# Performance work log

Measured on AMD Instinct MI355X. Metric: run time of the kernel, lower is better.

## Reference

```python
import jax, jax.numpy as jnp
import numpy as np

D_MODEL = 1024
N_HEADS = 16
D_FF = 4096
D_K = D_MODEL // N_HEADS


def _ln(x, g, b, eps=1e-5):
    mu = jnp.mean(x, axis=-1, keepdims=True)
    var = jnp.mean(jnp.square(x - mu), axis=-1, keepdims=True)
    return (x - mu) * jax.lax.rsqrt(var + eps) * g + b


def setup_inputs() -> dict:
    key = jax.random.key(0)
    ks = jax.random.split(key, 16)
    s = 0.02
    inp = {
        "x": jax.random.normal(ks[0], (2, 2048, D_MODEL), dtype=jnp.float32),
        "Wq": jax.random.normal(ks[1], (D_MODEL, D_MODEL), dtype=jnp.float32) * s,
        "bq": jnp.zeros((D_MODEL,), jnp.float32),
        "Wk": jax.random.normal(ks[2], (D_MODEL, D_MODEL), dtype=jnp.float32) * s,
        "bk": jnp.zeros((D_MODEL,), jnp.float32),
        "Wv": jax.random.normal(ks[3], (D_MODEL, D_MODEL), dtype=jnp.float32) * s,
        "bv": jnp.zeros((D_MODEL,), jnp.float32),
        "Wo": jax.random.normal(ks[4], (D_MODEL, D_MODEL), dtype=jnp.float32) * s,
        "bo": jnp.zeros((D_MODEL,), jnp.float32),
        "W1": jax.random.normal(ks[5], (D_MODEL, D_FF), dtype=jnp.float32) * s,
        "b1": jnp.zeros((D_FF,), jnp.float32),
        "W2": jax.random.normal(ks[6], (D_FF, D_MODEL), dtype=jnp.float32) * s,
        "b2": jnp.zeros((D_MODEL,), jnp.float32),
        "g1": jnp.ones((D_MODEL,), jnp.float32),
        "be1": jnp.zeros((D_MODEL,), jnp.float32),
        "g2": jnp.ones((D_MODEL,), jnp.float32),
        "be2": jnp.zeros((D_MODEL,), jnp.float32),
    }
    return inp


def reference(x, Wq, bq, Wk, bk, Wv, bv, Wo, bo, W1, b1, W2, b2, g1, be1, g2, be2):
    B, L, D = x.shape
    # QKV projections -> [B, H, L, d_k]
    q = (x @ Wq + bq).reshape(B, L, N_HEADS, D_K).transpose(0, 2, 1, 3)
    k = (x @ Wk + bk).reshape(B, L, N_HEADS, D_K).transpose(0, 2, 1, 3)
    v = (x @ Wv + bv).reshape(B, L, N_HEADS, D_K).transpose(0, 2, 1, 3)
    scores = jnp.einsum("bhqd,bhkd->bhqk", q, k) / jnp.sqrt(jnp.float32(D_K))
    attn = jax.nn.softmax(scores, axis=-1)
    ctx = jnp.einsum("bhqk,bhkd->bhqd", attn, v)
    ctx = ctx.transpose(0, 2, 1, 3).reshape(B, L, D)
    attn_out = ctx @ Wo + bo
    # residual + LN1
    h = _ln(x + attn_out, g1, be1)
    # FFN (exact GELU, matching torch F.gelu default)
    ff = jax.nn.gelu(h @ W1 + b1, approximate=False) @ W2 + b2
    return _ln(h + ff, g2, be2)
```

## Files before the change

kernel.cpp:

```cpp
#include <hip/hip_runtime.h>
#include <cmath>


typedef unsigned short u16;
typedef unsigned int u32;
typedef __attribute__((ext_vector_type(8))) __bf16 bf16x8;
typedef __attribute__((ext_vector_type(4))) float f32x4;

#define MFMA16(a, b, c) __builtin_amdgcn_mfma_f32_16x16x32_bf16(a, b, c, 0, 0, 0)

__device__ __forceinline__ u16 f2bf(float f) {
  u32 u = __builtin_bit_cast(u32, f);
  u += 0x7fffu + ((u >> 16) & 1u);
  return (u16)(u >> 16);
}

__device__ __forceinline__ u32 packtrunc(float lo, float hi) {
#if __has_builtin(__builtin_amdgcn_perm)
  return __builtin_amdgcn_perm(__builtin_bit_cast(u32, hi),
                               __builtin_bit_cast(u32, lo), 0x07060302u);
#else
  return (__builtin_bit_cast(u32, lo) >> 16) |
         (__builtin_bit_cast(u32, hi) & 0xFFFF0000u);
#endif
}

__device__ __forceinline__ bf16x8 ld_frag(const u16* p) {
  return __builtin_bit_cast(bf16x8, *(const uint4*)p);
}

__device__ __forceinline__ float fexp2(float x) {
#if __has_builtin(__builtin_amdgcn_exp2f)
  return __builtin_amdgcn_exp2f(x);
#else
  return exp2f(x);
#endif
}

__device__ __forceinline__ void gload16(const u16* g, u16* l) {
  __builtin_amdgcn_global_load_lds(
      (const __attribute__((address_space(1))) void*)g,
      (__attribute__((address_space(3))) void*)l, 16, 0, 0);
}

__global__ __launch_bounds__(256) void cvt_bf16_k(const float* __restrict__ src,
                                                  u16* __restrict__ dst) {
  int i = (blockIdx.x * 256 + threadIdx.x) * 4;
  float4 v = *(const float4*)(src + i);
  ushort4 o;
  o.x = f2bf(v.x); o.y = f2bf(v.y); o.z = f2bf(v.z); o.w = f2bf(v.w);
  *(ushort4*)(dst + i) = o;
}

__global__ __launch_bounds__(256) void transpose_bf16_k(const float* __restrict__ src,
                                                        u16* __restrict__ dst,
                                                        int R, int C) {
  __shared__ float tile[32][33];
  int tx = threadIdx.x & 31, ty = threadIdx.x >> 5;
  int c0 = blockIdx.x * 32, r0 = blockIdx.y * 32;
#pragma unroll
  for (int i = 0; i < 4; i++)
    tile[ty + 8 * i][tx] = src[(long)(r0 + ty + 8 * i) * C + c0 + tx];
  __syncthreads();
#pragma unroll
  for (int i = 0; i < 4; i++)
    dst[(long)(c0 + ty + 8 * i) * R + r0 + tx] = f2bf(tile[tx][ty + 8 * i]);
}

__global__ __launch_bounds__(256) void transpose4_bf16_k(
    const float* __restrict__ Wq, const float* __restrict__ Wk,
    const float* __restrict__ Wv, const float* __restrict__ Wo,
    u16* __restrict__ wqkvT, u16* __restrict__ woT) {
  const int z = blockIdx.z;
  const float* src = (z == 0) ? Wq : (z == 1) ? Wk : (z == 2) ? Wv : Wo;
  u16* dst = (z < 3) ? (wqkvT + (size_t)z * 1024 * 1024) : woT;
  __shared__ float tile[32][33];
  int tx = threadIdx.x & 31, ty = threadIdx.x >> 5;
  int c0 = blockIdx.x * 32, r0 = blockIdx.y * 32;
#pragma unroll
  for (int i = 0; i < 4; i++)
    tile[ty + 8 * i][tx] = src[(long)(r0 + ty + 8 * i) * 1024 + c0 + tx];
  __syncthreads();
#pragma unroll
  for (int i = 0; i < 4; i++)
    dst[(long)(c0 + ty + 8 * i) * 1024 + r0 + tx] = f2bf(tile[tx][ty + 8 * i]);
}

template <int MODE, int TN>
__global__ __launch_bounds__(256) void gemm_k(
    const u16* __restrict__ A, const u16* __restrict__ BT, int M, int N, int K,
    const float* __restrict__ bias, float* __restrict__ outF, u16* __restrict__ outB,
    u16* __restrict__ qd, u16* __restrict__ kd, u16* __restrict__ vTd,
    const float* __restrict__ bq, const float* __restrict__ bk, const float* __restrict__ bv) {
  constexpr int NT = TN / 32;
  __shared__ u16 As[2][128 * 32];
  __shared__ u16 Bs[2][TN * 32];
  const int tid = threadIdx.x;
  const int wave = tid >> 6, lane = tid & 63, quad = lane >> 4, l16 = lane & 15;
  const int wm = wave >> 1, wn = wave & 1;
  const int m0 = blockIdx.y * 128, n0 = blockIdx.x * TN;

  const int srow = lane >> 2;
  const int sxor = (lane & 3) ^ (srow & 3);
  const u16* aS0 = A + (long)(m0 + wave * 32 + srow) * K + sxor * 8;
  const u16* aS1 = aS0 + 16 * K;
  const u16* bS0 = BT + (long)(n0 + (TN == 128 ? wave * 32 : wave * 16) + srow) * K + sxor * 8;
  const u16* bS1 = bS0 + 16 * K;

  int aoff[4], boff[NT];
#pragma unroll
  for (int t = 0; t < 4; t++) {
    int ra = wm * 64 + t * 16 + l16;
    aoff[t] = ra * 32 + ((quad ^ (l16 & 3)) * 8);
  }
#pragma unroll
  for (int t = 0; t < NT; t++) {
    int rb = wn * (TN / 2) + t * 16 + l16;
    boff[t] = rb * 32 + ((quad ^ (l16 & 3)) * 8);
  }

  auto stage = [&](int buf, int k0) {
    gload16(aS0 + k0, &As[buf][(wave * 2 + 0) * 512]);
    gload16(aS1 + k0, &As[buf][(wave * 2 + 1) * 512]);
    if (TN == 128) {
      gload16(bS0 + k0, &Bs[buf][(wave * 2 + 0) * 512]);
      gload16(bS1 + k0, &Bs[buf][(wave * 2 + 1) * 512]);
    } else {
      gload16(bS0 + k0, &Bs[buf][wave * 512]);
    }
  };

  f32x4 acc[4][NT] = {};

  stage(0, 0);
#pragma unroll 1
  for (int k0 = 0; k0 < K; k0 += 32) {
    const int buf = (k0 >> 5) & 1;
    __syncthreads();
    if (k0 + 32 < K) stage(buf ^ 1, k0 + 32);
    bf16x8 af[4], bfr[NT];
#pragma unroll
    for (int t = 0; t < 4; t++) af[t] = ld_frag(&As[buf][aoff[t]]);
#pragma unroll
    for (int t = 0; t < NT; t++) bfr[t] = ld_frag(&Bs[buf][boff[t]]);
#pragma unroll
    for (int mt = 0; mt < 4; mt++)
#pragma unroll
      for (int nt = 0; nt < NT; nt++)
        acc[mt][nt] = MFMA16(af[mt], bfr[nt], acc[mt][nt]);
  }

  if (MODE == 0) {
    const int nbase = n0 + wn * (TN / 2);
    const int mat = nbase >> 10;
    const float* bp = (mat == 0) ? bq : ((mat == 1) ? bk : bv);
    float bb[NT];
    int hh0[NT], dd0[NT];
#pragma unroll
    for (int nt = 0; nt < NT; nt++) {
      int nn = (nbase + nt * 16 + l16) & 1023;
      bb[nt] = bp[nn];
      hh0[nt] = nn >> 6;
      dd0[nt] = nn & 63;
    }
    if (mat < 2) {
#pragma unroll
      for (int mt = 0; mt < 4; mt++) {
#pragma unroll
        for (int r = 0; r < 4; r++) {
          int mr = m0 + wm * 64 + mt * 16 + quad * 4 + r;
          int bI = mr >> 11, ll = mr & 2047;
#pragma unroll
          for (int nt = 0; nt < NT; nt++) {
            float v = acc[mt][nt][r] + bb[nt];
            long idx = ((long)((bI * 16 + hh0[nt]) * 2048 + ll)) * 64 + dd0[nt];
            if (mat == 0) {
              qd[idx] = f2bf(v * 0.18033688011112043f);
            } else {
              kd[idx] = f2bf(v);
            }
          }
        }
      }
    } else {
#pragma unroll
      for (int nt = 0; nt < NT; nt++) {
#pragma unroll
        for (int mt = 0; mt < 4; mt++) {
#pragma unroll
          for (int r = 0; r < 4; r++) {
            int mr = m0 + wm * 64 + mt * 16 + quad * 4 + r;
            int bI = mr >> 11, ll = mr & 2047;
            float v = acc[mt][nt][r] + bb[nt];
            vTd[((long)((bI * 16 + hh0[nt]) * 64 + dd0[nt])) * 2048 + ll] = f2bf(v);
          }
        }
      }
    }
  } else if (MODE == 1) {
    float bb[NT];
#pragma unroll
    for (int nt = 0; nt < NT; nt++) bb[nt] = bias[n0 + wn * (TN / 2) + nt * 16 + l16];
#pragma unroll
    for (int mt = 0; mt < 4; mt++) {
#pragma unroll
      for (int r = 0; r < 4; r++) {
        int mr = m0 + wm * 64 + mt * 16 + quad * 4 + r;
        float* orow = outF + (long)mr * N + n0 + wn * (TN / 2) + l16;
#pragma unroll
        for (int nt = 0; nt < NT; nt++)
          orow[nt * 16] = acc[mt][nt][r] + bb[nt];
      }
    }
  } else {
    float bb[NT];
#pragma unroll
    for (int nt = 0; nt < NT; nt++) bb[nt] = bias[n0 + wn * (TN / 2) + nt * 16 + l16];
#pragma unroll
    for (int mt = 0; mt < 4; mt++) {
#pragma unroll
      for (int r = 0; r < 4; r++) {
        int mr = m0 + wm * 64 + mt * 16 + quad * 4 + r;
        u16* orow = outB + (long)mr * N + n0 + wn * (TN / 2) + l16;
#pragma unroll
        for (int nt = 0; nt < NT; nt++) {
          float v = acc[mt][nt][r] + bb[nt];
          v = 0.5f * v * (1.0f + erff(v * 0.70710678118654752f));
          orow[nt * 16] = f2bf(v);
        }
      }
    }
  }
}

__global__ __launch_bounds__(256) void attn_k(const u16* __restrict__ qd,
                                              const u16* __restrict__ kd,
                                              const u16* __restrict__ vTd,
                                              u16* __restrict__ ctx) {
  __shared__ u16 Ks[2][64 * 64];
  __shared__ u16 Vs[2][64 * 64];
  __shared__ __align__(16) u16 P[4][32][72];
  const int tid = threadIdx.x;
  const int wave = tid >> 6, lane = tid & 63, quad = lane >> 4, l16 = lane & 15;
  const int bh = blockIdx.y;
  const u16* Q = qd + (long)bh * 2048 * 64;
  const u16* Kp = kd + (long)bh * 2048 * 64;
  const u16* Vt = vTd + (long)bh * 64 * 2048;
  const int qbase = blockIdx.x * 128 + wave * 32;

  bf16x8 qf[2][2];
#pragma unroll
  for (int qs = 0; qs < 2; qs++) {
    qf[qs][0] = ld_frag(Q + (qbase + qs * 16 + l16) * 64 + quad * 8);
    qf[qs][1] = ld_frag(Q + (qbase + qs * 16 + l16) * 64 + 32 + quad * 8);
  }

  f32x4 o[2][4] = {};
  float m[2] = {-1e30f, -1e30f}, l[2] = {0.f, 0.f};

  const int srow = lane >> 3;
  const int sx = (lane & 7) ^ srow;
  const int kr0 = wave * 16 + srow;
  const int kr1 = wave * 16 + 8 + srow;

  const int fs0 = ((0 * 4 + quad) ^ (l16 & 7)) * 8;
  const int fs1 = ((1 * 4 + quad) ^ (l16 & 7)) * 8;

  auto stage = [&](int buf, int j0) {
    gload16(Kp + (long)(j0 + kr0) * 64 + sx * 8, &Ks[buf][(wave * 2 + 0) * 512]);
    gload16(Kp + (long)(j0 + kr1) * 64 + sx * 8, &Ks[buf][(wave * 2 + 1) * 512]);
    gload16(Vt + (long)kr0 * 2048 + j0 + sx * 8, &Vs[buf][(wave * 2 + 0) * 512]);
    gload16(Vt + (long)kr1 * 2048 + j0 + sx * 8, &Vs[buf][(wave * 2 + 1) * 512]);
  };

  stage(0, 0);

#pragma unroll 1
  for (int j0 = 0; j0 < 2048; j0 += 64) {
    const int buf = (j0 >> 6) & 1;
    __syncthreads();
    if (j0 + 64 < 2048) stage(buf ^ 1, j0 + 64);

    const u16* kb = &Ks[buf][0];
    f32x4 st[2][4];
#pragma unroll
    for (int f = 0; f < 4; f++) {
      bf16x8 k0 = ld_frag(kb + (f * 16 + l16) * 64 + fs0);
      bf16x8 k1 = ld_frag(kb + (f * 16 + l16) * 64 + fs1);
      f32x4 s0 = {}, s1 = {};
      s0 = MFMA16(k0, qf[0][0], s0); s0 = MFMA16(k1, qf[0][1], s0);
      s1 = MFMA16(k0, qf[1][0], s1); s1 = MFMA16(k1, qf[1][1], s1);
      st[0][f] = s0; st[1][f] = s1;
    }

#pragma unroll
    for (int qs = 0; qs < 2; qs++) {
      float mx = -1e30f;
#pragma unroll
      for (int f = 0; f < 4; f++)
        mx = fmaxf(mx, fmaxf(fmaxf(st[qs][f][0], st[qs][f][1]),
                             fmaxf(st[qs][f][2], st[qs][f][3])));
      mx = fmaxf(mx, __shfl_xor(mx, 16));
      mx = fmaxf(mx, __shfl_xor(mx, 32));
      if (__ballot(mx > m[qs])) {
        float mn = fmaxf(m[qs], mx);
        float al = fexp2(m[qs] - mn);
        m[qs] = mn;
        l[qs] *= al;
#pragma unroll
        for (int nt = 0; nt < 4; nt++) {
          o[qs][nt][0] *= al; o[qs][nt][1] *= al;
          o[qs][nt][2] *= al; o[qs][nt][3] *= al;
        }
      }
      float sm = 0.f;
      u16* prow = &P[wave][qs * 16 + l16][0];
#pragma unroll
      for (int f = 0; f < 4; f++) {
        float p0 = fexp2(st[qs][f][0] - m[qs]);
        float p1 = fexp2(st[qs][f][1] - m[qs]);
        float p2 = fexp2(st[qs][f][2] - m[qs]);
        float p3 = fexp2(st[qs][f][3] - m[qs]);
        sm += (p0 + p1) + (p2 + p3);
        uint2 u;
        u.x = packtrunc(p0, p1);
        u.y = packtrunc(p2, p3);
        *(uint2*)(prow + f * 16 + quad * 4) = u;
      }
      sm += __shfl_xor(sm, 16);
      sm += __shfl_xor(sm, 32);
      l[qs] += sm;
    }
    __asm__ volatile("s_waitcnt lgkmcnt(0)" ::: "memory");

    const u16* vb = &Vs[buf][0];
    bf16x8 vf[4][2];
#pragma unroll
    for (int nt = 0; nt < 4; nt++) {
      vf[nt][0] = ld_frag(vb + (nt * 16 + l16) * 64 + fs0);
      vf[nt][1] = ld_frag(vb + (nt * 16 + l16) * 64 + fs1);
    }
#pragma unroll
    for (int qs = 0; qs < 2; qs++) {
      const u16* prow = &P[wave][qs * 16 + l16][0];
#pragma unroll
      for (int kh = 0; kh < 2; kh++) {
        bf16x8 pf = ld_frag(prow + kh * 32 + quad * 8);
#pragma unroll
        for (int nt = 0; nt < 4; nt++)
          o[qs][nt] = MFMA16(vf[nt][kh], pf, o[qs][nt]);
      }
    }
  }

  const int bI = bh >> 4, hh = bh & 15;
#pragma unroll
  for (int qs = 0; qs < 2; qs++) {
    const float rl = 1.0f / l[qs];
    const long row = (long)(bI * 2048 + qbase + qs * 16 + l16);
#pragma unroll
    for (int nt = 0; nt < 4; nt++) {
      ushort4 w;
      w.x = f2bf(o[qs][nt][0] * rl);
      w.y = f2bf(o[qs][nt][1] * rl);
      w.z = f2bf(o[qs][nt][2] * rl);
      w.w = f2bf(o[qs][nt][3] * rl);
      *(ushort4*)(ctx + row * 1024 + hh * 64 + nt * 16 + quad * 4) = w;
    }
  }
}

__global__ __launch_bounds__(256) void ln_k(const float* __restrict__ a,
                                            const float* __restrict__ b,
                                            const float* __restrict__ g,
                                            const float* __restrict__ be,
                                            float* __restrict__ outF,
                                            u16* __restrict__ outB) {
  const int row = blockIdx.x, tid = threadIdx.x;
  const float* pa = a + (long)row * 1024;
  const float* pb = b + (long)row * 1024;
  float v[4], s = 0.f, sq = 0.f;
#pragma unroll
  for (int i = 0; i < 4; i++) {
    int c = i * 256 + tid;
    v[i] = pa[c] + pb[c];
    s += v[i];
    sq += v[i] * v[i];
  }
#pragma unroll
  for (int off = 1; off < 64; off <<= 1) {
    s += __shfl_xor(s, off);
    sq += __shfl_xor(sq, off);
  }
  __shared__ float red[10];
  int wave = tid >> 6, lane = tid & 63;
  if (lane == 0) { red[wave * 2] = s; red[wave * 2 + 1] = sq; }
  __syncthreads();
  if (tid == 0) {
    float S = red[0] + red[2] + red[4] + red[6];
    float Q = red[1] + red[3] + red[5] + red[7];
    float mu = S * (1.0f / 1024.0f);
    float var = Q * (1.0f / 1024.0f) - mu * mu;
    red[8] = mu;
    red[9] = rsqrtf(var + 1e-5f);
  }
  __syncthreads();
  float mu = red[8], rstd = red[9];
#pragma unroll
  for (int i = 0; i < 4; i++) {
    int c = i * 256 + tid;
    float o = (v[i] - mu) * rstd * g[c] + be[c];
    outF[(long)row * 1024 + c] = o;
    if (outB) outB[(long)row * 1024 + c] = f2bf(o);
  }
}

extern "C" void kernel_launch(void* const* d_in, const int* in_sizes, int n_in,
                              void* d_out, int out_size, void* d_ws, size_t ws_size,
                              hipStream_t stream) {
  const float* x  = (const float*)d_in[0];
  const float* Wq = (const float*)d_in[1];  const float* bq = (const float*)d_in[2];
  const float* Wk = (const float*)d_in[3];  const float* bk = (const float*)d_in[4];
  const float* Wv = (const float*)d_in[5];  const float* bv = (const float*)d_in[6];
  const float* Wo = (const float*)d_in[7];  const float* bo = (const float*)d_in[8];
  const float* W1 = (const float*)d_in[9];  const float* b1 = (const float*)d_in[10];
  const float* W2 = (const float*)d_in[11]; const float* b2 = (const float*)d_in[12];
  const float* g1 = (const float*)d_in[13]; const float* be1 = (const float*)d_in[14];
  const float* g2 = (const float*)d_in[15]; const float* be2 = (const float*)d_in[16];

  char* ws = (char*)d_ws;
  size_t off = 0;
  auto alloc = [&](size_t bytes) {
    size_t o = off;
    off += (bytes + 255) & ~(size_t)255;
    return o;
  };
  u16*   xb     = (u16*)(ws + alloc(4096UL * 1024 * 2));
  u16*   wqkvT  = (u16*)(ws + alloc(3072UL * 1024 * 2));
  u16*   woT    = (u16*)(ws + alloc(1024UL * 1024 * 2));
  u16*   w1T    = (u16*)(ws + alloc(4096UL * 1024 * 2));
  u16*   w2T    = (u16*)(ws + alloc(1024UL * 4096 * 2));
  u16*   qb     = (u16*)(ws + alloc(32UL * 2048 * 64 * 2));
  u16*   kb     = (u16*)(ws + alloc(32UL * 2048 * 64 * 2));
  u16*   vTb    = (u16*)(ws + alloc(32UL * 64 * 2048 * 2));
  u16*   ctx    = (u16*)(ws + alloc(4096UL * 1024 * 2));
  float* attnO  = (float*)(ws + alloc(4096UL * 1024 * 4));
  float* h      = (float*)(ws + alloc(4096UL * 1024 * 4));
  u16*   hb     = (u16*)(ws + alloc(4096UL * 1024 * 2));
  u16*   ff1    = (u16*)(ws + alloc(4096UL * 4096 * 2));
  float* ff2    = (float*)(ws + alloc(4096UL * 1024 * 4));
  if (off > ws_size) return;

  cvt_bf16_k<<<4096, 256, 0, stream>>>(x, xb);
  transpose4_bf16_k<<<dim3(32, 32, 4), 256, 0, stream>>>(Wq, Wk, Wv, Wo, wqkvT, woT);
  transpose_bf16_k<<<dim3(128, 32), 256, 0, stream>>>(W1, w1T, 1024, 4096);
  transpose_bf16_k<<<dim3(32, 128), 256, 0, stream>>>(W2, w2T, 4096, 1024);

  gemm_k<0, 128><<<dim3(24, 32), 256, 0, stream>>>(xb, wqkvT, 4096, 3072, 1024,
                                                   nullptr, nullptr, nullptr,
                                                   qb, kb, vTb, bq, bk, bv);
  attn_k<<<dim3(16, 32), 256, 0, stream>>>(qb, kb, vTb, ctx);
  gemm_k<1, 64><<<dim3(16, 32), 256, 0, stream>>>(ctx, woT, 4096, 1024, 1024,
                                                  bo, attnO, nullptr,
                                                  nullptr, nullptr, nullptr, nullptr, nullptr, nullptr);
  ln_k<<<4096, 256, 0, stream>>>(x, attnO, g1, be1, h, hb);
  gemm_k<2, 128><<<dim3(32, 32), 256, 0, stream>>>(hb, w1T, 4096, 4096, 1024,
                                                   b1, nullptr, ff1,
                                                   nullptr, nullptr, nullptr, nullptr, nullptr, nullptr);
  gemm_k<1, 64><<<dim3(16, 32), 256, 0, stream>>>(ff1, w2T, 4096, 1024, 4096,
                                                  b2, ff2, nullptr,
                                                  nullptr, nullptr, nullptr, nullptr, nullptr, nullptr);
  ln_k<<<4096, 256, 0, stream>>>(h, ff2, g2, be2, (float*)d_out, nullptr);
}
```

Before: 418.9 us.

## Add 256x256 four-stage pipelined GEMM with split-K FFN2 and fused reduction LayerNorm

Adds a 512-thread GEMM kernel with 256x256 output tiles, a 4-deep LDS ring filled by direct global-to-LDS loads with explicit vmcnt waits, and interleaved stage/MFMA with priority bumps. It is used for the QKV projection and FFN1 to raise arithmetic intensity per tile. The FFN2 GEMM becomes split-K over 4 slices, writing partials into reused workspace buffers (ff2, attnO, qb, vTb). A new LayerNorm kernel sums the partials and the bias before normalising. This fixes the occupancy problem that a 4096x1024 output with large tiles would cause, at the cost of extra partial-sum memory traffic. Reusing qb and vTb as scratch relies on their sizes being sufficient.

```diff
diff --git a/kernel.cpp b/kernel.cpp
--- a/kernel.cpp
+++ b/kernel.cpp
@@ -42,6 +42,9 @@
       (const __attribute__((address_space(1))) void*)g,
       (__attribute__((address_space(3))) void*)l, 16, 0, 0);
 }
+
+#define WAITVL(N) asm volatile("s_waitcnt vmcnt(" #N ") lgkmcnt(0)" ::: "memory")
+#define BAR() do { __builtin_amdgcn_s_barrier(); asm volatile("" ::: "memory"); } while (0)
 
 __global__ __launch_bounds__(256) void cvt_bf16_k(const float* __restrict__ src,
                                                   u16* __restrict__ dst) {
@@ -84,6 +87,172 @@
 #pragma unroll
   for (int i = 0; i < 4; i++)
     dst[(long)(c0 + ty + 8 * i) * 1024 + r0 + tx] = f2bf(tile[tx][ty + 8 * i]);
+}
+
+template <int MODE>
+__global__ __launch_bounds__(512, 2) void gemm256_k(
+    const u16* __restrict__ A, const u16* __restrict__ BT,
+    int N, int lda, int ldb, int Kc,
+    const float* __restrict__ bias, float* __restrict__ outF, u16* __restrict__ outB,
+    float* __restrict__ p1, float* __restrict__ p2, float* __restrict__ p3,
+    u16* __restrict__ qd, u16* __restrict__ kd, u16* __restrict__ vTd,
+    const float* __restrict__ bq, const float* __restrict__ bk, const float* __restrict__ bv) {
+  __shared__ u16 As[4][256 * 32];
+  __shared__ u16 Bs[4][256 * 32];
+  const int tid = threadIdx.x;
+  const int wave = tid >> 6, lane = tid & 63, quad = lane >> 4, l16 = lane & 15;
+  const int wm = wave >> 2, wn = wave & 3;
+  const int m0 = blockIdx.y * 256, n0 = blockIdx.x * 256;
+  const int kz = blockIdx.z;
+  const long kofs = (long)kz * Kc;
+  const int KT = Kc >> 5;
+
+  const int srow = lane >> 2;
+  const int sseg = (lane & 3) ^ (srow & 3);
+  const u16* aS = A + (long)(m0 + wave * 32 + srow) * lda + kofs + sseg * 8;
+  const u16* bS = BT + (long)(n0 + wave * 32 + srow) * ldb + kofs + sseg * 8;
+
+  auto stageA = [&](int sb, int s) {
+    const u16* p = aS + (long)s * 32;
+    gload16(p, &As[sb][wave * 1024]);
+    gload16(p + 16 * (long)lda, &As[sb][wave * 1024 + 512]);
+  };
+  auto stageB = [&](int sb, int s) {
+    const u16* p = bS + (long)s * 32;
+    gload16(p, &Bs[sb][wave * 1024]);
+    gload16(p + 16 * (long)ldb, &Bs[sb][wave * 1024 + 512]);
+  };
+
+  int aro[8], bro[4];
+#pragma unroll
+  for (int mf = 0; mf < 8; mf++) {
+    int r = wm * 128 + mf * 16 + l16;
+    aro[mf] = r * 32 + ((quad ^ (r & 3)) * 8);
+  }
+#pragma unroll
+  for (int nf = 0; nf < 4; nf++) {
+    int r = wn * 64 + nf * 16 + l16;
+    bro[nf] = r * 32 + ((quad ^ (r & 3)) * 8);
+  }
+
+  f32x4 acc[8][4] = {};
+
+  stageA(0, 0); stageB(0, 0);
+  stageA(1, 1); stageB(1, 1);
+  stageA(2, 2); stageB(2, 2);
+
+#pragma unroll 1
+  for (int t = 0; t < KT; ++t) {
+    const int buf = t & 3;
+    if (t < KT - 2)      { WAITVL(8); }
+    else if (t == KT - 2){ WAITVL(4); }
+    else                 { WAITVL(0); }
+    BAR();
+
+    if (t + 3 < KT) stageA((t + 3) & 3, t + 3);
+    bf16x8 af[4], bf4[4];
+#pragma unroll
+    for (int i = 0; i < 4; i++) af[i] = ld_frag(&As[buf][aro[i]]);
+#pragma unroll
+    for (int i = 0; i < 4; i++) bf4[i] = ld_frag(&Bs[buf][bro[i]]);
+    __builtin_amdgcn_s_setprio(1);
+#pragma unroll
+    for (int mf = 0; mf < 4; mf++)
+#pragma unroll
+      for (int nf = 0; nf < 4; nf++)
+        acc[mf][nf] = MFMA16(af[mf], bf4[nf], acc[mf][nf]);
+    __builtin_amdgcn_s_setprio(0);
+
+    if (t + 3 < KT) stageB((t + 3) & 3, t + 3);
+#pragma unroll
+    for (int i = 0; i < 4; i++) af[i] = ld_frag(&As[buf][aro[4 + i]]);
+    __builtin_amdgcn_s_setprio(1);
+#pragma unroll
+    for (int mf = 0; mf < 4; mf++)
+#pragma unroll
+      for (int nf = 0; nf < 4; nf++)
+        acc[4 + mf][nf] = MFMA16(af[mf], bf4[nf], acc[4 + mf][nf]);
+    __builtin_amdgcn_s_setprio(0);
+  }
+
+  if (MODE == 0) {
+    const int nbase = n0 + wn * 64;
+    const int mat = nbase >> 10;
+    const float* bp = (mat == 0) ? bq : ((mat == 1) ? bk : bv);
+    float bb[4];
+    int hh0[4], dd0[4];
+#pragma unroll
+    for (int nf = 0; nf < 4; nf++) {
+      int nn = (nbase + nf * 16 + l16) & 1023;
+      bb[nf] = bp[nn];
+      hh0[nf] = nn >> 6;
+      dd0[nf] = nn & 63;
+    }
+    if (mat < 2) {
+#pragma unroll
+      for (int mf = 0; mf < 8; mf++) {
+#pragma unroll
+        for (int r = 0; r < 4; r++) {
+          int mr = m0 + wm * 128 + mf * 16 + quad * 4 + r;
+          int bI = mr >> 11, ll = mr & 2047;
+#pragma unroll
+          for (int nf = 0; nf < 4; nf++) {
+            float v = acc[mf][nf][r] + bb[nf];
+            long idx = ((long)((bI * 16 + hh0[nf]) * 2048 + ll)) * 64 + dd0[nf];
+            if (mat == 0) {
+              qd[idx] = f2bf(v * 0.18033688011112043f);
+            } else {
+              kd[idx] = f2bf(v);
+            }
+          }
+        }
+      }
+    } else {
+#pragma unroll
+      for (int nf = 0; nf < 4; nf++) {
+#pragma unroll
+        for (int mf = 0; mf < 8; mf++) {
+#pragma unroll
+          for (int r = 0; r < 4; r++) {
+            int mr = m0 + wm * 128 + mf * 16 + quad * 4 + r;
+            int bI = mr >> 11, ll = mr & 2047;
+            float v = acc[mf][nf][r] + bb[nf];
+            vTd[((long)((bI * 16 + hh0[nf]) * 64 + dd0[nf])) * 2048 + ll] = f2bf(v);
+          }
+        }
+      }
+    }
+  } else if (MODE == 2) {
+    float bb[4];
+#pragma unroll
+    for (int nf = 0; nf < 4; nf++) bb[nf] = bias[n0 + wn * 64 + nf * 16 + l16];
+#pragma unroll
+    for (int mf = 0; mf < 8; mf++) {
+#pragma unroll
+      for (int r = 0; r < 4; r++) {
+        int mr = m0 + wm * 128 + mf * 16 + quad * 4 + r;
+        u16* orow = outB + (long)mr * N + n0 + wn * 64 + l16;
+#pragma unroll
+        for (int nf = 0; nf < 4; nf++) {
+          float v = acc[mf][nf][r] + bb[nf];
+          v = 0.5f * v * (1.0f + erff(v * 0.70710678118654752f));
+          orow[nf * 16] = f2bf(v);
+        }
+      }
+    }
+  } else {
+    float* sl = (kz == 0) ? outF : (kz == 1) ? p1 : (kz == 2) ? p2 : p3;
+#pragma unroll
+    for (int mf = 0; mf < 8; mf++) {
+#pragma unroll
+      for (int r = 0; r < 4; r++) {
+        int mr = m0 + wm * 128 + mf * 16 + quad * 4 + r;
+        float* orow = sl + (long)mr * N + n0 + wn * 64 + l16;
+#pragma unroll
+        for (int nf = 0; nf < 4; nf++) orow[nf * 16] = acc[mf][nf][r];
+      }
+    }
+  }
 }
 
 template <int MODE, int TN>
@@ -150,54 +319,7 @@
         acc[mt][nt] = MFMA16(af[mt], bfr[nt], acc[mt][nt]);
   }
 
-  if (MODE == 0) {
-    const int nbase = n0 + wn * (TN / 2);
-    const int mat = nbase >> 10;
-    const float* bp = (mat == 0) ? bq : ((mat == 1) ? bk : bv);
-    float bb[NT];
-    int hh0[NT], dd0[NT];
-#pragma unroll
-    for (int nt = 0; nt < NT; nt++) {
-      int nn = (nbase + nt * 16 + l16) & 1023;
-      bb[nt] = bp[nn];
-      hh0[nt] = nn >> 6;
-      dd0[nt] = nn & 63;
-    }
-    if (mat < 2) {
-#pragma unroll
-      for (int mt = 0; mt < 4; mt++) {
-#pragma unroll
-        for (int r = 0; r < 4; r++) {
-          int mr = m0 + wm * 64 + mt * 16 + quad * 4 + r;
-          int bI = mr >> 11, ll = mr & 2047;
-#pragma unroll
-          for (int nt = 0; nt < NT; nt++) {
-            float v = acc[mt][nt][r] + bb[nt];
-            long idx = ((long)((bI * 16 + hh0[nt]) * 2048 + ll)) * 64 + dd0[nt];
-            if (mat == 0) {
-              qd[idx] = f2bf(v * 0.18033688011112043f);
-            } else {
-              kd[idx] = f2bf(v);
-            }
-          }
-        }
-      }
-    } else {
-#pragma unroll
-      for (int nt = 0; nt < NT; nt++) {
-#pragma unroll
-        for (int mt = 0; mt < 4; mt++) {
-#pragma unroll
-          for (int r = 0; r < 4; r++) {
-            int mr = m0 + wm * 64 + mt * 16 + quad * 4 + r;
-            int bI = mr >> 11, ll = mr & 2047;
-            float v = acc[mt][nt][r] + bb[nt];
-            vTd[((long)((bI * 16 + hh0[nt]) * 64 + dd0[nt])) * 2048 + ll] = f2bf(v);
-          }
-        }
-      }
-    }
-  } else if (MODE == 1) {
+  if (MODE == 1) {
     float bb[NT];
 #pragma unroll
     for (int nt = 0; nt < NT; nt++) bb[nt] = bias[n0 + wn * (TN / 2) + nt * 16 + l16];
@@ -210,24 +332,6 @@
 #pragma unroll
         for (int nt = 0; nt < NT; nt++)
           orow[nt * 16] = acc[mt][nt][r] + bb[nt];
-      }
-    }
-  } else {
-    float bb[NT];
-#pragma unroll
-    for (int nt = 0; nt < NT; nt++) bb[nt] = bias[n0 + wn * (TN / 2) + nt * 16 + l16];
-#pragma unroll
-    for (int mt = 0; mt < 4; mt++) {
-#pragma unroll
-      for (int r = 0; r < 4; r++) {
-        int mr = m0 + wm * 64 + mt * 16 + quad * 4 + r;
-        u16* orow = outB + (long)mr * N + n0 + wn * (TN / 2) + l16;
-#pragma unroll
-        for (int nt = 0; nt < NT; nt++) {
-          float v = acc[mt][nt][r] + bb[nt];
-          v = 0.5f * v * (1.0f + erff(v * 0.70710678118654752f));
-          orow[nt * 16] = f2bf(v);
-        }
       }
     }
   }
@@ -412,6 +516,52 @@
     float o = (v[i] - mu) * rstd * g[c] + be[c];
     outF[(long)row * 1024 + c] = o;
     if (outB) outB[(long)row * 1024 + c] = f2bf(o);
+  }
+}
+
+__global__ __launch_bounds__(256) void ln4_k(const float* __restrict__ a,
+                                             const float* __restrict__ q0,
+                                             const float* __restrict__ q1,
+                                             const float* __restrict__ q2,
+                                             const float* __restrict__ q3,
+                                             const float* __restrict__ bias,
+                                             const float* __restrict__ g,
+                                             const float* __restrict__ be,
+                                             float* __restrict__ outF) {
+  const int row = blockIdx.x, tid = threadIdx.x;
+  const long base = (long)row * 1024;
+  float v[4], s = 0.f, sq = 0.f;
+#pragma unroll
+  for (int i = 0; i < 4; i++) {
+    int c = i * 256 + tid;
+    float ff = (q0[base + c] + q1[base + c]) + (q2[base + c] + q3[base + c]) + bias[c];
+    v[i] = a[base + c] + ff;
+    s += v[i];
+    sq += v[i] * v[i];
+  }
+#pragma unroll
+  for (int off = 1; off < 64; off <<= 1) {
+    s += __shfl_xor(s, off);
+    sq += __shfl_xor(sq, off);
+  }
+  __shared__ float red[10];
+  int wave = tid >> 6, lane = tid & 63;
+  if (lane == 0) { red[wave * 2] = s; red[wave * 2 + 1] = sq; }
+  __syncthreads();
+  if (tid == 0) {
+    float S = red[0] + red[2] + red[4] + red[6];
+    float Q = red[1] + red[3] + red[5] + red[7];
+    float mu = S * (1.0f / 1024.0f);
+    float var = Q * (1.0f / 1024.0f) - mu * mu;
+    red[8] = mu;
+    red[9] = rsqrtf(var + 1e-5f);
+  }
+  __syncthreads();
+  float mu = red[8], rstd = red[9];
+#pragma unroll
+  for (int i = 0; i < 4; i++) {
+    int c = i * 256 + tid;
+    outF[base + c] = (v[i] - mu) * rstd * g[c] + be[c];
   }
 }
 
@@ -451,24 +601,32 @@
   float* ff2    = (float*)(ws + alloc(4096UL * 1024 * 4));
   if (off > ws_size) return;
 
+  float* sl0 = ff2;
+  float* sl1 = attnO;
+  float* sl2 = (float*)qb;
+  float* sl3 = (float*)vTb;
+
   cvt_bf16_k<<<4096, 256, 0, stream>>>(x, xb);
   transpose4_bf16_k<<<dim3(32, 32, 4), 256, 0, stream>>>(Wq, Wk, Wv, Wo, wqkvT, woT);
   transpose_bf16_k<<<dim3(128, 32), 256, 0, stream>>>(W1, w1T, 1024, 4096);
   transpose_bf16_k<<<dim3(32, 128), 256, 0, stream>>>(W2, w2T, 4096, 1024);
 
-  gemm_k<0, 128><<<dim3(24, 32), 256, 0, stream>>>(xb, wqkvT, 4096, 3072, 1024,
-                                                   nullptr, nullptr, nullptr,
-                                                   qb, kb, vTb, bq, bk, bv);
+  gemm256_k<0><<<dim3(12, 16), 512, 0, stream>>>(
+      xb, wqkvT, 3072, 1024, 1024, 1024,
+      nullptr, nullptr, nullptr, nullptr, nullptr, nullptr,
+      qb, kb, vTb, bq, bk, bv);
   attn_k<<<dim3(16, 32), 256, 0, stream>>>(qb, kb, vTb, ctx);
   gemm_k<1, 64><<<dim3(16, 32), 256, 0, stream>>>(ctx, woT, 4096, 1024, 1024,
                                                   bo, attnO, nullptr,
                                                   nullptr, nullptr, nullptr, nullptr, nullptr, nullptr);
   ln_k<<<4096, 256, 0, stream>>>(x, attnO, g1, be1, h, hb);
-  gemm_k<2, 128><<<dim3(32, 32), 256, 0, stream>>>(hb, w1T, 4096, 4096, 1024,
-                                                   b1, nullptr, ff1,
-                                                   nullptr, nullptr, nullptr, nullptr, nullptr, nullptr);
-  gemm_k<1, 64><<<dim3(16, 32), 256, 0, stream>>>(ff1, w2T, 4096, 1024, 4096,
-                                                  b2, ff2, nullptr,
-                                                  nullptr, nullptr, nullptr, nullptr, nullptr, nullptr);
-  ln_k<<<4096, 256, 0, stream>>>(h, ff2, g2, be2, (float*)d_out, nullptr);
-}
+  gemm256_k<2><<<dim3(16, 16), 512, 0, stream>>>(
+      hb, w1T, 4096, 1024, 1024, 1024,
+      b1, nullptr, ff1, nullptr, nullptr, nullptr,
+      nullptr, nullptr, nullptr, nullptr, nullptr, nullptr);
+  gemm256_k<3><<<dim3(4, 16, 4), 512, 0, stream>>>(
+      ff1, w2T, 1024, 4096, 4096, 1024,
+      nullptr, sl0, nullptr, sl1, sl2, sl3,
+      nullptr, nullptr, nullptr, nullptr, nullptr, nullptr);
+  ln4_k<<<4096, 256, 0, stream>>>(h, sl0, sl1, sl2, sl3, b2, g2, be2, (float*)d_out);
+}
```

Result: no change. 411.5 us (-1.8%).
